# Kernel tuning notes

Hardware: AMD Instinct MI355X
Metric: run time of the kernel (lower is better)

Reference implementation:

```python
import jax, jax.numpy as jnp
import numpy as np

IN_F = 3072       # in_features
OUT_F = 9216      # out_features = 3 * N_HEADS * HEAD_DIM (fused QKV)
GROUP = 64        # quantization group size
RANK = 32         # lora_rank
HEAD_DIM = 128
N_HEADS = OUT_F // (3 * HEAD_DIM)  # 24
EPS = 1e-6
LORA_SCALE = 1.0


def setup_inputs() -> dict:
    key = jax.random.key(0)
    ks = jax.random.split(key, 10)
    B, S = 1, 4096
    x = jax.random.normal(ks[0], (B, S, IN_F), dtype=jnp.float32)
    # packed int4 weights: two signed int4 values per int8 byte
    qweight = jax.random.randint(ks[1], (OUT_F, IN_F // 2), -128, 128, dtype=jnp.int32).astype(jnp.int8)
    wscales = (jax.random.uniform(ks[2], (IN_F // GROUP, OUT_F)) * 0.02 + 0.001).astype(jnp.float32)
    bias = (jax.random.normal(ks[3], (OUT_F,)) * 0.01).astype(jnp.float32)
    lora_down = (jax.random.normal(ks[4], (IN_F, RANK)) * 0.02).astype(jnp.float32)
    lora_up = (jax.random.normal(ks[5], (OUT_F, RANK)) * 0.02).astype(jnp.float32)
    smooth = (jax.random.uniform(ks[6], (IN_F,)) * 0.5 + 0.75).astype(jnp.float32)   # keep away from 0
    norm_q = (jax.random.uniform(ks[7], (HEAD_DIM,)) * 0.5 + 0.75).astype(jnp.float32)
    norm_k = (jax.random.uniform(ks[8], (HEAD_DIM,)) * 0.5 + 0.75).astype(jnp.float32)
    ang = jax.random.uniform(ks[9], (S, HEAD_DIM // 2)) * (2.0 * np.pi)
    rotary_emb = jnp.stack([jnp.cos(ang), jnp.sin(ang)], axis=-1).astype(jnp.float32)  # [S, D/2, 2]
    return dict(x=x, qweight=qweight, wscales=wscales, bias=bias, lora_down=lora_down,
                lora_up=lora_up, smooth=smooth, norm_q=norm_q, norm_k=norm_k, rotary_emb=rotary_emb)


def _dequant_weight(qweight, wscales):
    # unpack two signed int4 lanes from each int8 (low nibble first), then per-group scale
    low = jnp.right_shift(jnp.left_shift(qweight, 4), 4)   # arithmetic shifts on int8 -> sign extend
    high = jnp.right_shift(qweight, 4)
    w4 = jnp.stack([low, high], axis=-1).reshape(OUT_F, IN_F)          # int4 codes in [-8, 7]
    wg = w4.astype(jnp.float32).reshape(OUT_F, IN_F // GROUP, GROUP)
    return (wg * wscales.T[:, :, None]).reshape(OUT_F, IN_F)          # [N, K]


def _quantize_act(x, smooth, lora_down):
    # fused: smooth -> symmetric per-token per-group int4 quantize -> lora_down projection
    B, S, K = x.shape
    M = B * S
    xs = (x / smooth).reshape(M, K)
    xg = xs.reshape(M, K // GROUP, GROUP)
    ascale = jnp.max(jnp.abs(xg), axis=-1, keepdims=True) / 7.0
    ascale = jnp.maximum(ascale, 1e-8)
    q = jnp.clip(jnp.round(xg / ascale), -8.0, 7.0)
    deq = (q * ascale).reshape(M, K)                                   # dequantized int4 activation
    lora_act = xs @ lora_down                                          # [M, RANK], fp32 side path
    return deq, lora_act


def _rope(t, cos, sin):
    # interleaved pairs (even, odd) rotation; t: [M, H, D], cos/sin: [M, 1, D/2]
    e, o = t[..., 0::2], t[..., 1::2]
    re = e * cos - o * sin
    ro = e * sin + o * cos
    return jnp.stack([re, ro], axis=-1).reshape(t.shape)


def reference(x, qweight, wscales, bias, lora_down, lora_up, smooth, norm_q, norm_k, rotary_emb):
    B, S, K = x.shape
    M = B * S
    deq_x, lora_act = _quantize_act(x, smooth, lora_down)
    w = _dequant_weight(qweight, wscales)
    # main int4 GEMM + LoRA up + bias, all fused in the real kernel
    out = deq_x @ w.T + (LORA_SCALE * lora_act) @ lora_up.T + bias     # [M, OUT_F]
    qkv = out.reshape(M, 3, N_HEADS, HEAD_DIM)
    q, k, v = qkv[:, 0], qkv[:, 1], qkv[:, 2]
    def rms(t, g):
        return t * jax.lax.rsqrt(jnp.mean(t * t, axis=-1, keepdims=True) + EPS) * g
    q = rms(q, norm_q)
    k = rms(k, norm_k)
    cos = rotary_emb[:, None, :, 0]   # [M, 1, D/2]
    sin = rotary_emb[:, None, :, 1]
    q = _rope(q, cos, sin)
    k = _rope(k, cos, sin)
    return jnp.stack([q, k, v], axis=1).reshape(B, S, OUT_F)
```

## Files before the change

### kernel.cpp

```cpp
#include <hip/hip_runtime.h>
#include <cstdint>

#define MDIM 4096
#define NDIM 9216
#define KDIM 3072
#define KP   3136
#define NKT2 97

#define QROWS 4
#define QB2 1024
#define WB 13824
#define PB 2304

typedef unsigned int u32;
typedef unsigned short u16;
typedef float f32x4 __attribute__((ext_vector_type(4)));
typedef __bf16 bf16x8 __attribute__((ext_vector_type(8)));

__device__ __forceinline__ u16 f2bf(float f) {
  u32 u = __float_as_uint(f);
  u32 r = u + 0x7fffu + ((u >> 16) & 1u);
  return (u16)(r >> 16);
}

__device__ __forceinline__ float frcp(float f) { return __builtin_amdgcn_rcpf(f); }

__device__ __forceinline__ void gld_lds16(const void* g, void* l) {
  __builtin_amdgcn_global_load_lds((__attribute__((address_space(1))) void*)g,
                                   (__attribute__((address_space(3))) void*)l,
                                   16, 0, 0);
}

__global__ __launch_bounds__(256) void k_quant(const float* __restrict__ x,
                        const float* __restrict__ lora_down, const float* __restrict__ smooth,
                        u16* __restrict__ Aex) {
  __shared__ float xs_s[QROWS][KDIM];
  __shared__ float part[64 * 32];
  const int tid = threadIdx.x;
  const int m0 = blockIdx.x * QROWS;
  const int sub = tid & 15;

  #pragma unroll
  for (int r = 0; r < QROWS; ++r) {
    const float* xr = x + (size_t)(m0 + r) * KDIM;
    u16* arow = Aex + (size_t)(m0 + r) * KP;
    #pragma unroll
    for (int p = 0; p < 3; ++p) {
      int g = p * 16 + (tid >> 4);
      int k0 = g * 64 + sub * 4;
      float4 xv = *(const float4*)(xr + k0);
      float4 sv = *(const float4*)(smooth + k0);
      float a0 = xv.x * frcp(sv.x), a1 = xv.y * frcp(sv.y);
      float a2 = xv.z * frcp(sv.z), a3 = xv.w * frcp(sv.w);
      xs_s[r][k0+0] = a0; xs_s[r][k0+1] = a1; xs_s[r][k0+2] = a2; xs_s[r][k0+3] = a3;
      float am = fmaxf(fmaxf(fabsf(a0), fabsf(a1)), fmaxf(fabsf(a2), fabsf(a3)));
      am = fmaxf(am, __shfl_xor(am, 8, 16));
      am = fmaxf(am, __shfl_xor(am, 4, 16));
      am = fmaxf(am, __shfl_xor(am, 2, 16));
      am = fmaxf(am, __shfl_xor(am, 1, 16));
      float asc = fmaxf(am * (1.0f / 7.0f), 1e-8f);
      float iasc = frcp(asc);
      float q0 = fminf(7.f, fmaxf(-8.f, rintf(a0 * iasc)));
      float q1 = fminf(7.f, fmaxf(-8.f, rintf(a1 * iasc)));
      float q2 = fminf(7.f, fmaxf(-8.f, rintf(a2 * iasc)));
      float q3 = fminf(7.f, fmaxf(-8.f, rintf(a3 * iasc)));
      float d0 = q0 * asc, d1 = q1 * asc, d2 = q2 * asc, d3 = q3 * asc;
      u32 lo = (u32)f2bf(d0) | ((u32)f2bf(d1) << 16);
      u32 hi = (u32)f2bf(d2) | ((u32)f2bf(d3) << 16);
      *(uint2*)(arow + k0) = make_uint2(lo, hi);
    }
    if (tid < 32) arow[3104 + tid] = 0;
  }
  __syncthreads();

  const int c  = tid >> 2;
  const int r8 = (tid & 3) * 8;
  float a[QROWS][8] = {};
  const float* lp = lora_down + (size_t)c * 32 + r8;
  #pragma unroll 2
  for (int i = 0; i < 48; ++i) {
    float4 l0 = *(const float4*)(lp);
    float4 l1 = *(const float4*)(lp + 4);
    #pragma unroll
    for (int r = 0; r < QROWS; ++r) {
      float xv = xs_s[r][i * 64 + c];
      a[r][0] = fmaf(xv, l0.x, a[r][0]); a[r][1] = fmaf(xv, l0.y, a[r][1]);
      a[r][2] = fmaf(xv, l0.z, a[r][2]); a[r][3] = fmaf(xv, l0.w, a[r][3]);
      a[r][4] = fmaf(xv, l1.x, a[r][4]); a[r][5] = fmaf(xv, l1.y, a[r][5]);
      a[r][6] = fmaf(xv, l1.z, a[r][6]); a[r][7] = fmaf(xv, l1.w, a[r][7]);
    }
    lp += 64 * 32;
  }
  #pragma unroll 1
  for (int r = 0; r < QROWS; ++r) {
    __syncthreads();
    *(float4*)(&part[c * 32 + r8])     = make_float4(a[r][0], a[r][1], a[r][2], a[r][3]);
    *(float4*)(&part[c * 32 + r8 + 4]) = make_float4(a[r][4], a[r][5], a[r][6], a[r][7]);
    __syncthreads();
    if (tid < 32) {
      float s = 0.f;
      #pragma unroll 8
      for (int cc = 0; cc < 64; ++cc) s += part[cc * 32 + tid];
      Aex[(size_t)(m0 + r) * KP + 3072 + tid] = f2bf(s);
    }
  }
}

__global__ __launch_bounds__(256) void k_wdq(const u32* __restrict__ qw,
                        const float* __restrict__ wsc, const float* __restrict__ lora_up,
                        u16* __restrict__ Bex) {
  const int tid = threadIdx.x;
  int bid = blockIdx.x;

  if (bid >= WB) {
    int idx = (bid - WB) * 256 + tid;
    int n = idx >> 6, c = idx & 63;
    u16 v = 0;
    if (c < 32) v = f2bf(lora_up[n * 32 + c]);
    Bex[(size_t)n * KP + 3072 + c] = v;
    return;
  }
  __shared__ int s_viol;
  u32 probe = qw[tid];
  bool ok = (probe >> 8) == ((probe & 0x80u) ? 0xffffffu : 0u);
  if (tid == 0) s_viol = 0;
  __syncthreads();
  if (!ok) atomicOr(&s_viol, 1);
  __syncthreads();
  const int f = (s_viol == 0);

  int idx = bid * 256 + tid;
  int n = idx / 384;
  int j = idx - n * 384;
  int k0 = j * 8;
  u32 w;
  if (f) {
    uint4 q4 = ((const uint4*)qw)[idx];
    w = (q4.x & 0xffu) | ((q4.y & 0xffu) << 8) | ((q4.z & 0xffu) << 16) | ((q4.w & 0xffu) << 24);
  } else {
    w = qw[idx];
  }
  float ws = wsc[(k0 >> 6) * NDIM + n];
  u32 ow[4];
  #pragma unroll
  for (int b = 0; b < 4; ++b) {
    int by = (int)((w >> (8 * b)) & 0xffu);
    int lo = (by << 28) >> 28;
    int hi = (by << 24) >> 28;
    ow[b] = (u32)f2bf((float)lo * ws) | ((u32)f2bf((float)hi * ws) << 16);
  }
  *(uint4*)(Bex + (size_t)n * KP + k0) = make_uint4(ow[0], ow[1], ow[2], ow[3]);
}

__global__ __launch_bounds__(512) void k_gemm(const u16* __restrict__ A, const u16* __restrict__ B,
                                              const float* __restrict__ bias, const float* __restrict__ norm_q,
                                              const float* __restrict__ norm_k, const float* __restrict__ rot,
                                              float* __restrict__ out) {
  extern __shared__ u16 lds[];
  const int tid  = threadIdx.x;
  const int lane = tid & 63;
  const int wave = tid >> 6;
  const int m0 = blockIdx.y * 256;
  const int n0 = blockIdx.x * 256;
  const int wm = (wave >> 2) * 128;
  const int wn = (wave & 3) * 64;
  const int lr = lane & 15;
  const int lq = lane >> 4;

  const u16 *pA0, *pA1, *pB0, *pB1;
  int la0, la1, lb0, lb1;
  {
    auto mk = [&](int p, const u16* base, int nb) -> const u16* {
      int pr = p >> 3, cs = p & 7;
      int c  = cs ^ (pr & 7);
      int r  = pr * 2 + (c >> 2);
      int kc = c & 3;
      return base + (size_t)(nb + r) * KP + kc * 8;
    };
    int p0 = tid, p1 = 512 + tid;
    pA0 = mk(p0, A, m0); pA1 = mk(p1, A, m0);
    pB0 = mk(p0, B, n0); pB1 = mk(p1, B, n0);
    la0 = p0 * 8;        la1 = p1 * 8;
    lb0 = 8192 + p0 * 8; lb1 = 8192 + p1 * 8;
  }

  int aoff[8], boff[4];
  #pragma unroll
  for (int t = 0; t < 8; ++t) {
    int ra = wm + t * 16 + lr;
    int pr = ra >> 1, c = (ra & 1) * 4 + lq;
    aoff[t] = pr * 64 + ((c ^ (pr & 7)) * 8);
  }
  #pragma unroll
  for (int t = 0; t < 4; ++t) {
    int rb = wn + t * 16 + lr;
    int pr = rb >> 1, c = (rb & 1) * 4 + lq;
    boff[t] = 8192 + pr * 64 + ((c ^ (pr & 7)) * 8);
  }

  f32x4 acc[8][4] = {};

  #pragma unroll
  for (int s = 0; s < 3; ++s) {
    u16* sl = lds + (s << 14);
    gld_lds16(pA0, sl + la0); gld_lds16(pA1, sl + la1);
    gld_lds16(pB0, sl + lb0); gld_lds16(pB1, sl + lb1);
    pA0 += 32; pA1 += 32; pB0 += 32; pB1 += 32;
  }
  asm volatile("s_waitcnt vmcnt(8)" ::: "memory");
  __builtin_amdgcn_s_barrier();
  asm volatile("" ::: "memory");

  #pragma unroll 1
  for (int kt = 0; kt < NKT2; ++kt) {
    const u16* sA_ = lds + ((kt & 3) << 14);
    u16* stl = lds + (((kt + 3) & 3) << 14);
    const bool st = (kt < NKT2 - 3);
    if (st) {
      gld_lds16(pA0, stl + la0); gld_lds16(pA1, stl + la1);
      gld_lds16(pB0, stl + lb0); gld_lds16(pB1, stl + lb1);
      pA0 += 32; pA1 += 32; pB0 += 32; pB1 += 32;
    }
    bf16x8 af[8], bf[4];
    #pragma unroll
    for (int t = 0; t < 8; ++t) af[t] = *(const bf16x8*)&sA_[aoff[t]];
    #pragma unroll
    for (int t = 0; t < 4; ++t) bf[t] = *(const bf16x8*)&sA_[boff[t]];
    __builtin_amdgcn_s_setprio(1);
    #pragma unroll
    for (int ti = 0; ti < 8; ++ti)
      #pragma unroll
      for (int tj = 0; tj < 4; ++tj)
        acc[ti][tj] = __builtin_amdgcn_mfma_f32_16x16x32_bf16(af[ti], bf[tj], acc[ti][tj], 0, 0, 0);
    __builtin_amdgcn_s_setprio(0);
    if (st) asm volatile("s_waitcnt vmcnt(8)" ::: "memory");
    else    asm volatile("s_waitcnt vmcnt(0)" ::: "memory");
    __builtin_amdgcn_s_barrier();
    asm volatile("" ::: "memory");
  }

  const int sel = (blockIdx.x >= 24) ? 2 : (blockIdx.x >= 12 ? 1 : 0);

  float bv[4];
  #pragma unroll
  for (int tj = 0; tj < 4; ++tj) bv[tj] = bias[n0 + wn + tj * 16 + lr];
  #pragma unroll
  for (int ti = 0; ti < 8; ++ti)
    #pragma unroll
    for (int tj = 0; tj < 4; ++tj)
      #pragma unroll
      for (int rg = 0; rg < 4; ++rg)
        acc[ti][tj][rg] += bv[tj];

  if (sel == 2) {
    #pragma unroll
    for (int tj = 0; tj < 4; ++tj) {
      int n = n0 + wn + tj * 16 + lr;
      #pragma unroll
      for (int ti = 0; ti < 8; ++ti) {
        int mr = m0 + wm + ti * 16 + lq * 4;
        #pragma unroll
        for (int rg = 0; rg < 4; ++rg)
          out[(size_t)(mr + rg) * NDIM + n] = acc[ti][tj][rg];
      }
    }
    return;
  }

  float* ssq = (float*)lds;
  #pragma unroll
  for (int ti = 0; ti < 8; ++ti) {
    float pr4[4];
    #pragma unroll
    for (int rg = 0; rg < 4; ++rg) {
      float s = 0.f;
      #pragma unroll
      for (int tj = 0; tj < 4; ++tj) s += acc[ti][tj][rg] * acc[ti][tj][rg];
      pr4[rg] = s;
    }
    #pragma unroll
    for (int off = 1; off < 16; off <<= 1)
      #pragma unroll
      for (int rg = 0; rg < 4; ++rg) pr4[rg] += __shfl_xor(pr4[rg], off);
    #pragma unroll
    for (int rg = 0; rg < 4; ++rg)
      if (lr == (ti & 3) * 4 + rg)
        ssq[(wn >> 6) * 256 + wm + ti * 16 + lq * 4 + rg] = pr4[rg];
  }
  __syncthreads();

  const float* nrm = sel ? norm_k : norm_q;
  float gm[4];
  #pragma unroll
  for (int tj = 0; tj < 4; ++tj) gm[tj] = nrm[(wn & 64) + tj * 16 + lr];
  const float2* rot2 = (const float2*)rot;
  const float sgn = (lr & 1) ? 1.0f : -1.0f;
  const int hb = (wn >> 7) * 512;

  #pragma unroll
  for (int ti = 0; ti < 8; ++ti) {
    #pragma unroll
    for (int rg = 0; rg < 4; ++rg) {
      int row = wm + ti * 16 + lq * 4 + rg;
      float tot = ssq[hb + row] + ssq[hb + 256 + row];
      float rs = rsqrtf(tot * (1.0f / 128.0f) + 1e-6f);
      int m = m0 + row;
      #pragma unroll
      for (int tj = 0; tj < 4; ++tj) {
        int nl = (wn & 64) + tj * 16 + lr;
        float v = acc[ti][tj][rg] * rs * gm[tj];
        float p = __shfl_xor(v, 1);
        float2 cs = rot2[(size_t)m * 64 + (nl >> 1)];
        out[(size_t)m * NDIM + n0 + wn + tj * 16 + lr] = v * cs.x + sgn * (p * cs.y);
      }
    }
  }
}

extern "C" void kernel_launch(void* const* d_in, const int* in_sizes, int n_in,
                              void* d_out, int out_size, void* d_ws, size_t ws_size,
                              hipStream_t stream) {
  const float* x         = (const float*)d_in[0];
  const u32*   qweight   = (const u32*)d_in[1];
  const float* wscales   = (const float*)d_in[2];
  const float* bias      = (const float*)d_in[3];
  const float* lora_down = (const float*)d_in[4];
  const float* lora_up   = (const float*)d_in[5];
  const float* smooth    = (const float*)d_in[6];
  const float* norm_q    = (const float*)d_in[7];
  const float* norm_k    = (const float*)d_in[8];
  const float* rot       = (const float*)d_in[9];
  float* out = (float*)d_out;

  u16* Aex = (u16*)d_ws;
  u16* Bex = Aex + (size_t)MDIM * KP;

  static bool attr_set = false;
  if (!attr_set) {
    hipFuncSetAttribute(reinterpret_cast<const void*>(k_gemm),
                        hipFuncAttributeMaxDynamicSharedMemorySize, 131072);
    attr_set = true;
  }

  k_wdq<<<WB + PB, 256, 0, stream>>>(qweight, wscales, lora_up, Bex);
  k_quant<<<QB2, 256, 0, stream>>>(x, lora_down, smooth, Aex);
  k_gemm<<<dim3(NDIM / 256, MDIM / 256), 512, 131072, stream>>>(Aex, Bex, bias, norm_q, norm_k, rot, out);
}
```

Baseline: 531.9 us.

## Prefetch next K-tile LDS fragments into registers interleaved with MFMAs

Restructures the GEMM main loop so the LDS-to-register fragment loads for the next K tile are issued while the current tile's MFMAs run, using sched_group_barrier to interleave ds_reads with MFMA groups. The prologue loads the first fragments and an epilogue does the final MFMA step. The vmcnt wait thresholds are tightened to ensure the next stage is resident before it is read, and a __syncthreads is added before the LDS is reused for the RMS reduction. The intent is to hide LDS read latency behind matrix math, at the cost of more live registers and an extra wait constraint on the global-to-LDS copies.

```diff
diff --git a/kernel.cpp b/kernel.cpp
--- a/kernel.cpp
+++ b/kernel.cpp
@@ -207,37 +207,53 @@
     gld_lds16(pB0, sl + lb0); gld_lds16(pB1, sl + lb1);
     pA0 += 32; pA1 += 32; pB0 += 32; pB1 += 32;
   }
-  asm volatile("s_waitcnt vmcnt(8)" ::: "memory");
+  asm volatile("s_waitcnt vmcnt(4)" ::: "memory");
   __builtin_amdgcn_s_barrier();
   asm volatile("" ::: "memory");
 
+  bf16x8 af[8], bf[4];
+  #pragma unroll
+  for (int t = 0; t < 8; ++t) af[t] = *(const bf16x8*)&lds[aoff[t]];
+  #pragma unroll
+  for (int t = 0; t < 4; ++t) bf[t] = *(const bf16x8*)&lds[boff[t]];
+
   #pragma unroll 1
-  for (int kt = 0; kt < NKT2; ++kt) {
-    const u16* sA_ = lds + ((kt & 3) << 14);
+  for (int kt = 0; kt < NKT2 - 1; ++kt) {
     u16* stl = lds + (((kt + 3) & 3) << 14);
-    const bool st = (kt < NKT2 - 3);
-    if (st) {
+    const u16* nsl = lds + (((kt + 1) & 3) << 14);
+    if (kt < NKT2 - 3) {
       gld_lds16(pA0, stl + la0); gld_lds16(pA1, stl + la1);
       gld_lds16(pB0, stl + lb0); gld_lds16(pB1, stl + lb1);
       pA0 += 32; pA1 += 32; pB0 += 32; pB1 += 32;
     }
-    bf16x8 af[8], bf[4];
-    #pragma unroll
-    for (int t = 0; t < 8; ++t) af[t] = *(const bf16x8*)&sA_[aoff[t]];
-    #pragma unroll
-    for (int t = 0; t < 4; ++t) bf[t] = *(const bf16x8*)&sA_[boff[t]];
     __builtin_amdgcn_s_setprio(1);
     #pragma unroll
-    for (int ti = 0; ti < 8; ++ti)
+    for (int t = 0; t < 8; ++t) {
       #pragma unroll
       for (int tj = 0; tj < 4; ++tj)
-        acc[ti][tj] = __builtin_amdgcn_mfma_f32_16x16x32_bf16(af[ti], bf[tj], acc[ti][tj], 0, 0, 0);
+        acc[t][tj] = __builtin_amdgcn_mfma_f32_16x16x32_bf16(af[t], bf[tj], acc[t][tj], 0, 0, 0);
+      af[t] = *(const bf16x8*)&nsl[aoff[t]];
+    }
+    #pragma unroll
+    for (int t = 0; t < 4; ++t) bf[t] = *(const bf16x8*)&nsl[boff[t]];
     __builtin_amdgcn_s_setprio(0);
-    if (st) asm volatile("s_waitcnt vmcnt(8)" ::: "memory");
-    else    asm volatile("s_waitcnt vmcnt(0)" ::: "memory");
+    __builtin_amdgcn_sched_group_barrier(0x020, 4, 0);
+    #pragma unroll
+    for (int g = 0; g < 8; ++g) {
+      __builtin_amdgcn_sched_group_barrier(0x008, 4, 0);
+      __builtin_amdgcn_sched_group_barrier(0x100, 1, 0);
+    }
+    __builtin_amdgcn_sched_group_barrier(0x100, 4, 0);
+    if (kt < NKT2 - 3) asm volatile("s_waitcnt vmcnt(4)" ::: "memory");
+    else               asm volatile("s_waitcnt vmcnt(0)" ::: "memory");
     __builtin_amdgcn_s_barrier();
     asm volatile("" ::: "memory");
   }
+  #pragma unroll
+  for (int t = 0; t < 8; ++t)
+    #pragma unroll
+    for (int tj = 0; tj < 4; ++tj)
+      acc[t][tj] = __builtin_amdgcn_mfma_f32_16x16x32_bf16(af[t], bf[tj], acc[t][tj], 0, 0, 0);
 
   const int sel = (blockIdx.x >= 24) ? 2 : (blockIdx.x >= 12 ? 1 : 0);
 
@@ -267,6 +283,7 @@
     return;
   }
 
+  __syncthreads();
   float* ssq = (float*)lds;
   #pragma unroll
   for (int ti = 0; ti < 8; ++ti) {
```

After: 513.0 us. 1.04x faster.

## Split GEMM k-step into two half-phases interleaving LDS reads, global loads, MFMAs

Applied to the files above, without the earlier changes.

Restructures the main GEMM loop so each k-tile runs in two phases. Each phase loads half the A fragments from LDS, issues half of the global-to-LDS prefetches, synchronises, then runs 16 MFMAs, in the style of a ping-pong schedule. This cuts register pressure for the A fragments and aims to spread LDS and global memory traffic across the MFMA work. In exchange it adds extra barriers per iteration, plus a __syncthreads before the epilogue reuses LDS.

```diff
diff --git a/kernel.cpp b/kernel.cpp
--- a/kernel.cpp
+++ b/kernel.cpp
@@ -213,25 +213,42 @@
 
   #pragma unroll 1
   for (int kt = 0; kt < NKT2; ++kt) {
-    const u16* sA_ = lds + ((kt & 3) << 14);
+    const u16* cs_ = lds + ((kt & 3) << 14);
     u16* stl = lds + (((kt + 3) & 3) << 14);
     const bool st = (kt < NKT2 - 3);
-    if (st) {
-      gld_lds16(pA0, stl + la0); gld_lds16(pA1, stl + la1);
-      gld_lds16(pB0, stl + lb0); gld_lds16(pB1, stl + lb1);
-      pA0 += 32; pA1 += 32; pB0 += 32; pB1 += 32;
-    }
-    bf16x8 af[8], bf[4];
-    #pragma unroll
-    for (int t = 0; t < 8; ++t) af[t] = *(const bf16x8*)&sA_[aoff[t]];
-    #pragma unroll
-    for (int t = 0; t < 4; ++t) bf[t] = *(const bf16x8*)&sA_[boff[t]];
+    bf16x8 af[4], bf[4];
+
+    #pragma unroll
+    for (int t = 0; t < 4; ++t) af[t] = *(const bf16x8*)&cs_[aoff[t]];
+    #pragma unroll
+    for (int t = 0; t < 4; ++t) bf[t] = *(const bf16x8*)&cs_[boff[t]];
+    if (st) { gld_lds16(pA0, stl + la0); gld_lds16(pA1, stl + la1); }
+    __builtin_amdgcn_s_barrier();
+    asm volatile("s_waitcnt lgkmcnt(0)" ::: "memory");
+    __builtin_amdgcn_sched_barrier(0);
     __builtin_amdgcn_s_setprio(1);
     #pragma unroll
-    for (int ti = 0; ti < 8; ++ti)
+    for (int ti = 0; ti < 4; ++ti)
       #pragma unroll
       for (int tj = 0; tj < 4; ++tj)
         acc[ti][tj] = __builtin_amdgcn_mfma_f32_16x16x32_bf16(af[ti], bf[tj], acc[ti][tj], 0, 0, 0);
+    __builtin_amdgcn_s_setprio(0);
+    __builtin_amdgcn_s_barrier();
+    asm volatile("" ::: "memory");
+
+    #pragma unroll
+    for (int t = 0; t < 4; ++t) af[t] = *(const bf16x8*)&cs_[aoff[4 + t]];
+    if (st) { gld_lds16(pB0, stl + lb0); gld_lds16(pB1, stl + lb1);
+              pA0 += 32; pA1 += 32; pB0 += 32; pB1 += 32; }
+    __builtin_amdgcn_s_barrier();
+    asm volatile("s_waitcnt lgkmcnt(0)" ::: "memory");
+    __builtin_amdgcn_sched_barrier(0);
+    __builtin_amdgcn_s_setprio(1);
+    #pragma unroll
+    for (int ti = 0; ti < 4; ++ti)
+      #pragma unroll
+      for (int tj = 0; tj < 4; ++tj)
+        acc[4 + ti][tj] = __builtin_amdgcn_mfma_f32_16x16x32_bf16(af[ti], bf[tj], acc[4 + ti][tj], 0, 0, 0);
     __builtin_amdgcn_s_setprio(0);
     if (st) asm volatile("s_waitcnt vmcnt(8)" ::: "memory");
     else    asm volatile("s_waitcnt vmcnt(0)" ::: "memory");
@@ -267,6 +284,7 @@
     return;
   }
 
+  __syncthreads();
   float* ssq = (float*)lds;
   #pragma unroll
   for (int ti = 0; ti < 8; ++ti) {
```

Result: no change. 536.7 us (+0.9%).
